# Kernel tuning notes

Measured on AMD Instinct MI355X. Metric: run time of the kernel, lower is better.

## Reference

```python
import jax, jax.numpy as jnp
import numpy as np

D_MODEL = 512
N_HEAD = 8
D_HEAD = D_MODEL // N_HEAD


def setup_inputs() -> dict:
    key = jax.random.key(0)
    ks = jax.random.split(key, 8)
    B, S, T = 4, 512, 32
    src = jax.random.normal(ks[0], (B, S, D_MODEL), dtype=jnp.float32)
    tgt = jax.random.normal(ks[1], (B, S, T, D_MODEL), dtype=jnp.float32)
    tgt_padding_mask = jax.random.bernoulli(ks[2], 0.1, (B, S, T))
    scale = 1.0 / np.sqrt(D_MODEL)
    in_proj_weight = jax.random.uniform(ks[3], (3 * D_MODEL, D_MODEL), dtype=jnp.float32, minval=-scale, maxval=scale)
    in_proj_bias = jnp.zeros((3 * D_MODEL,), dtype=jnp.float32)
    out_proj_weight = jax.random.uniform(ks[4], (D_MODEL, D_MODEL), dtype=jnp.float32, minval=-scale, maxval=scale)
    out_proj_bias = jnp.zeros((D_MODEL,), dtype=jnp.float32)
    return {
        "src": src,
        "tgt": tgt,
        "tgt_padding_mask": tgt_padding_mask,
        "in_proj_weight": in_proj_weight,
        "in_proj_bias": in_proj_bias,
        "out_proj_weight": out_proj_weight,
        "out_proj_bias": out_proj_bias,
    }


def reference(src, tgt, tgt_padding_mask, in_proj_weight, in_proj_bias, out_proj_weight, out_proj_bias):
    # KNN-style cross attention branch (tgt is [B, S, T, D]).
    B, S, _ = src.shape
    T = tgt.shape[-2]
    w_src, w_tgt = in_proj_weight[:D_MODEL], in_proj_weight[D_MODEL:]
    b_src, b_tgt = in_proj_bias[:D_MODEL], in_proj_bias[D_MODEL:]

    q = src @ w_src.T + b_src                      # [B, S, D]
    kv = tgt @ w_tgt.T + b_tgt                     # [B, S, T, 2D]
    k, v = kv[..., :D_MODEL], kv[..., D_MODEL:]

    # mask handling: drop the mask for queries with no valid tgt, zero them later
    attn_invalid = tgt_padding_mask                # [B, S, T]
    mask_no_tgt_valid = jnp.all(attn_invalid, axis=-1)           # [B, S]
    attn_invalid = attn_invalid & ~mask_no_tgt_valid[..., None]

    q = q.reshape(B, S, N_HEAD, D_HEAD)            # [B, S, H, Dh]
    k = k.reshape(B, S, T, N_HEAD, D_HEAD)
    v = v.reshape(B, S, T, N_HEAD, D_HEAD)

    attn = jnp.einsum("bshd,bsthd->bhst", q, k)    # [B, H, S, T]
    attn = jnp.where(attn_invalid[:, None], -jnp.inf, attn)
    attn = jax.nn.softmax(attn / jnp.sqrt(jnp.asarray(D_HEAD, attn.dtype)), axis=-1)

    out = jnp.einsum("bhst,bsthd->bshd", attn, v).reshape(B, S, D_MODEL)
    out = out @ out_proj_weight.T + out_proj_bias
    out = jnp.where(mask_no_tgt_valid[..., None], 0.0, out)
    return out
```

## Files before the change

kernel.cpp:

```cpp
#include <hip/hip_runtime.h>
#include <hip/hip_bf16.h>


typedef __attribute__((ext_vector_type(8))) short frag8;
typedef __attribute__((ext_vector_type(4))) float f32x4;

__device__ __forceinline__ short f2s(float v) {
    return __builtin_bit_cast(short, __float2bfloat16(v));
}
__device__ __forceinline__ float s2f(short x) {
    return __builtin_bit_cast(float, (unsigned)(unsigned short)x << 16);
}
__device__ __forceinline__ void stv(float* p, float v)          { *p = v; }
__device__ __forceinline__ void stv(__hip_bfloat16* p, float v) { *p = __float2bfloat16(v); }

__device__ __forceinline__ void gl_lds16(const __hip_bfloat16* g, __hip_bfloat16* l) {
    __builtin_amdgcn_global_load_lds(
        (const __attribute__((address_space(1))) unsigned int*)g,
        (__attribute__((address_space(3))) unsigned int*)l, 16, 0, 0);
}

__global__ __launch_bounds__(256)
void k_prep(const float* __restrict__ ipw, const float* __restrict__ opw,
            const float* __restrict__ src,
            __hip_bfloat16* __restrict__ ipw_bf, __hip_bfloat16* __restrict__ opw_bf,
            __hip_bfloat16* __restrict__ src_bf, __hip_bfloat16* __restrict__ Tk)
{
    __shared__ short tile[64][65];
    int b = blockIdx.x, tid = threadIdx.x;
#pragma unroll
    for (int i = 0; i < 4; ++i) {
        int g = b * 1024 + i * 256 + tid;
        const float4* in; ushort4* o4; int off;
        if (g < 196608)      { in = (const float4*)ipw; o4 = (ushort4*)ipw_bf; off = g; }
        else if (g < 262144) { in = (const float4*)opw; o4 = (ushort4*)opw_bf; off = g - 196608; }
        else                 { in = (const float4*)src; o4 = (ushort4*)src_bf; off = g - 262144; }
        float4 v = in[off];
        ushort4 o;
        o.x = (unsigned short)f2s(v.x); o.y = (unsigned short)f2s(v.y);
        o.z = (unsigned short)f2s(v.z); o.w = (unsigned short)f2s(v.w);
        o4[off] = o;
    }
    if (b < 128) {
        int bx = b & 15, by = b >> 4;
        const float* sp = ipw + (size_t)512 * 512;
#pragma unroll
        for (int i = 0; i < 16; ++i) {
            int idx = i * 256 + tid;
            int r = idx >> 6, c = idx & 63;
            tile[r][c] = f2s(sp[(size_t)(bx * 64 + r) * 512 + by * 64 + c]);
        }
        __syncthreads();
        short* Tks = (short*)Tk;
#pragma unroll
        for (int i = 0; i < 16; ++i) {
            int idx = i * 256 + tid;
            int rr = idx >> 6, cc = idx & 63;
            Tks[(size_t)(by * 64 + rr) * 1024 + bx * 64 + cc] = tile[cc][rr];
        }
    }
}

template<typename OUTT>
__device__ __forceinline__
void gemm64_dev(const __hip_bfloat16* __restrict__ A, const __hip_bfloat16* __restrict__ W,
                const float* __restrict__ bias, OUTT* __restrict__ C,
                const int* __restrict__ zmask,
                int N, int K, int tm, int tn, char* smem, int tid)
{
    short* sA = (short*)smem;
    short* sB = sA + 4096;
    int lane = tid & 63, w = tid >> 6;
    int wm = w >> 1, wn = w & 1;
    const __hip_bfloat16* Ab = A + (size_t)tm * 64 * K;
    const __hip_bfloat16* Wb = W + (size_t)tn * 64 * K;

    f32x4 acc[2][2];
#pragma unroll
    for (int i = 0; i < 2; ++i)
#pragma unroll
        for (int j = 0; j < 2; ++j) acc[i][j] = {0.f, 0.f, 0.f, 0.f};

    int wbase = (tid & ~63) * 8;
    int m = lane & 15, q = lane >> 4;
    int sw = (m & 7) * 8;
    int trow = tid >> 3;
    int tcb  = ((tid & 7) ^ (trow & 7)) * 8;

    for (int k0 = 0; k0 < K; k0 += 64) {
        gl_lds16(Ab + (size_t)trow * K + k0 + tcb,        (__hip_bfloat16*)&sA[wbase]);
        gl_lds16(Ab + (size_t)(32 + trow) * K + k0 + tcb, (__hip_bfloat16*)&sA[2048 + wbase]);
        gl_lds16(Wb + (size_t)trow * K + k0 + tcb,        (__hip_bfloat16*)&sB[wbase]);
        gl_lds16(Wb + (size_t)(32 + trow) * K + k0 + tcb, (__hip_bfloat16*)&sB[2048 + wbase]);
        __syncthreads();
#pragma unroll
        for (int ki = 0; ki < 2; ++ki) {
            frag8 af[2], bf2[2];
#pragma unroll
            for (int i = 0; i < 2; ++i)
                af[i] = *(const frag8*)&sA[(wm * 32 + i * 16 + m) * 64 + ((ki * 32 + q * 8) ^ sw)];
#pragma unroll
            for (int j = 0; j < 2; ++j)
                bf2[j] = *(const frag8*)&sB[(wn * 32 + j * 16 + m) * 64 + ((ki * 32 + q * 8) ^ sw)];
#pragma unroll
            for (int i = 0; i < 2; ++i)
#pragma unroll
                for (int j = 0; j < 2; ++j)
                    acc[i][j] = __builtin_amdgcn_mfma_f32_16x16x32_bf16(
                        af[i], bf2[j], acc[i][j], 0, 0, 0);
        }
        __syncthreads();
    }

    int rb = q * 4;
    bool zr[2][4] = {{false,false,false,false},{false,false,false,false}};
    if (zmask) {
#pragma unroll
        for (int i = 0; i < 2; ++i)
#pragma unroll
            for (int t = 0; t < 4; ++t) {
                int row = tm * 64 + wm * 32 + i * 16 + rb + t;
                const uint4* mp = (const uint4*)(zmask + (size_t)row * 32);
                unsigned a = 0xffffffffu;
#pragma unroll
                for (int u = 0; u < 8; ++u) { uint4 v = mp[u]; a &= v.x & v.y & v.z & v.w; }
                zr[i][t] = (a != 0u);
            }
    }
#pragma unroll
    for (int j = 0; j < 2; ++j) {
        int   col = tn * 64 + wn * 32 + j * 16 + m;
        float bv  = bias[col];
#pragma unroll
        for (int i = 0; i < 2; ++i) {
            int row0 = tm * 64 + wm * 32 + i * 16 + rb;
#pragma unroll
            for (int t = 0; t < 4; ++t) {
                float v = acc[i][j][t] + bv;
                if (zr[i][t]) v = 0.f;
                stv(&C[(size_t)(row0 + t) * N + col], v);
            }
        }
    }
}

__device__ __forceinline__
void gemm_bt_wave(const __hip_bfloat16* __restrict__ A, int lda,
                  const __hip_bfloat16* __restrict__ W, int ldw,
                  const float* __restrict__ bias, int bc0,
                  __hip_bfloat16* __restrict__ C, int ldc,
                  int K, int tm, int tn, int lane)
{
    int r  = lane & 15;
    int kq = (lane >> 4) << 3;
    const __hip_bfloat16* Ap = A + (size_t)(tm * 32 + r) * lda + kq;
    const __hip_bfloat16* Wp = W + (size_t)(tn * 32 + r) * ldw + kq;

    f32x4 acc[2][2];
#pragma unroll
    for (int i = 0; i < 2; ++i)
#pragma unroll
        for (int j = 0; j < 2; ++j) acc[i][j] = {0.f, 0.f, 0.f, 0.f};

    for (int k0 = 0; k0 < K; k0 += 32) {
        frag8 a[2], b[2];
#pragma unroll
        for (int i = 0; i < 2; ++i) a[i] = *(const frag8*)(Ap + (size_t)i * 16 * lda + k0);
#pragma unroll
        for (int j = 0; j < 2; ++j) b[j] = *(const frag8*)(Wp + (size_t)j * 16 * ldw + k0);
#pragma unroll
        for (int i = 0; i < 2; ++i)
#pragma unroll
            for (int j = 0; j < 2; ++j)
                acc[i][j] = __builtin_amdgcn_mfma_f32_16x16x32_bf16(a[i], b[j], acc[i][j], 0, 0, 0);
    }

    int rb = (lane >> 4) * 4;
#pragma unroll
    for (int j = 0; j < 2; ++j) {
        int   col = tn * 32 + j * 16 + r;
        float bv  = bias ? bias[bc0 + col] : 0.f;
#pragma unroll
        for (int i = 0; i < 2; ++i) {
            int row0 = tm * 32 + i * 16 + rb;
#pragma unroll
            for (int t = 0; t < 4; ++t)
                C[(size_t)(row0 + t) * ldc + col] = __float2bfloat16(acc[i][j][t] + bv);
        }
    }
}

__global__ __launch_bounds__(256)
void k_q(const __hip_bfloat16* src_bf, const __hip_bfloat16* ipw_bf,
         const float* ipb, __hip_bfloat16* q_bf)
{
    __shared__ __align__(16) char smem[16384];
    int b = blockIdx.x;
    gemm64_dev<__hip_bfloat16>(src_bf, ipw_bf, ipb, q_bf, nullptr,
                               512, 512, b >> 3, b & 7, smem, threadIdx.x);
}

__global__ __launch_bounds__(256)
void k_qk(const __hip_bfloat16* q_bf, const __hip_bfloat16* Tk, __hip_bfloat16* qkh)
{
    int tid = threadIdx.x;
    int t = blockIdx.x * 4 + (tid >> 6);
    int z = t >> 10, loc = t & 1023;
    gemm_bt_wave(q_bf + z * 64, 512, Tk + z * 64, 1024, nullptr, 0,
                 qkh + (size_t)z * 512, 4096, 64, loc >> 4, loc & 15, tid & 63);
}

__global__ __launch_bounds__(256)
void k_attn(const float* __restrict__ tgt,
            const __hip_bfloat16* __restrict__ qkh,
            const int* __restrict__ mask,
            __hip_bfloat16* __restrict__ tbar)
{
    int bs   = blockIdx.x;
    int tid  = threadIdx.x;
    int lane = tid & 63;
    int wv   = tid >> 6;
    int m    = lane & 15;
    int g4   = lane >> 4;

    __shared__ short sS[32 * 520];
    __shared__ short sQK[8 * 520];
    __shared__ int   sM[32];

    const float* tg = tgt + (size_t)bs * 32 * 512;
#pragma unroll
    for (int i = 0; i < 16; ++i) {
        int idx = i * 256 + tid;
        int row = idx >> 7, c4 = (idx & 127) * 4;
        float4 v = *(const float4*)(tg + (size_t)row * 512 + c4);
        ushort4 o;
        o.x = (unsigned short)f2s(v.x); o.y = (unsigned short)f2s(v.y);
        o.z = (unsigned short)f2s(v.z); o.w = (unsigned short)f2s(v.w);
        *(ushort4*)&sS[row * 520 + c4] = o;
    }
    const ushort4* qk4 = (const ushort4*)(qkh + (size_t)bs * 4096);
#pragma unroll
    for (int i = 0; i < 4; ++i) {
        int u = i * 256 + tid;
        int h = u >> 7, c4 = (u & 127) * 4;
        *(ushort4*)&sQK[h * 520 + c4] = qk4[u];
    }
    if (tid < 32) sM[tid] = mask[bs * 32 + tid];
    __syncthreads();

    int mk0 = sM[m], mk1 = sM[16 + m];
    bool allm = __all((mk0 != 0) && (mk1 != 0));

    f32x4 acc0 = {0.f,0.f,0.f,0.f}, acc1 = {0.f,0.f,0.f,0.f};
    {
        const short* qb  = &sQK[(m & 7) * 520 + g4 * 8];
        const short* t0p = &sS[m * 520 + g4 * 8];
        const short* t1p = t0p + 16 * 520;
#pragma unroll
        for (int k0 = 0; k0 < 512; k0 += 32) {
            frag8 af = *(const frag8*)(qb + k0);
            frag8 b0 = *(const frag8*)(t0p + k0);
            frag8 b1 = *(const frag8*)(t1p + k0);
            acc0 = __builtin_amdgcn_mfma_f32_16x16x32_bf16(af, b0, acc0, 0, 0, 0);
            acc1 = __builtin_amdgcn_mfma_f32_16x16x32_bf16(af, b1, acc1, 0, 0, 0);
        }
    }

    float p0v[4], p1v[4];
#pragma unroll
    for (int r = 0; r < 4; ++r) {
        float s0 = acc0[r] * 0.125f, s1 = acc1[r] * 0.125f;
        if (!allm) {
            if (mk0) s0 = -__builtin_inff();
            if (mk1) s1 = -__builtin_inff();
        }
        float mx = fmaxf(s0, s1);
#pragma unroll
        for (int off = 1; off < 16; off <<= 1) mx = fmaxf(mx, __shfl_xor(mx, off));
        float e0 = __expf(s0 - mx), e1 = __expf(s1 - mx);
        float sm = e0 + e1;
#pragma unroll
        for (int off = 1; off < 16; off <<= 1) sm += __shfl_xor(sm, off);
        float inv = 1.f / sm;
        p0v[r] = e0 * inv; p1v[r] = e1 * inv;
    }
    __syncthreads();

    short* sPw = sQK + wv * 512;
    if (g4 < 2) {
#pragma unroll
        for (int r = 0; r < 4; ++r) {
            int h = g4 * 4 + r;
            short h0 = f2s(p0v[r]), h1 = f2s(p1v[r]);
            sPw[h * 32 + m]            = h0;
            sPw[h * 32 + 16 + m]       = h1;
            sPw[256 + h * 32 + m]      = f2s(p0v[r] - s2f(h0));
            sPw[256 + h * 32 + 16 + m] = f2s(p1v[r] - s2f(h1));
        }
    }
    __syncthreads();
    frag8 paH = *(const frag8*)(sPw + (m & 7) * 32 + g4 * 8);
    frag8 paL = *(const frag8*)(sPw + 256 + (m & 7) * 32 + g4 * 8);
    __syncthreads();

    short* sO = sQK;
#pragma unroll
    for (int ci = 0; ci < 8; ++ci) {
        int cg = wv * 8 + ci;
        int cbase = cg * 16 + m;
        frag8 vb;
#pragma unroll
        for (int j = 0; j < 8; ++j)
            vb[j] = sS[(g4 * 8 + j) * 520 + cbase];
        f32x4 d = {0.f,0.f,0.f,0.f};
        d = __builtin_amdgcn_mfma_f32_16x16x32_bf16(paH, vb, d, 0, 0, 0);
        d = __builtin_amdgcn_mfma_f32_16x16x32_bf16(paL, vb, d, 0, 0, 0);
        if (g4 < 2) {
#pragma unroll
            for (int r = 0; r < 4; ++r)
                sO[(g4 * 4 + r) * 512 + cg * 16 + m] = f2s(d[r]);
        }
    }
    __syncthreads();

    ushort4* dst = (ushort4*)(tbar + (size_t)bs * 4096);
    const ushort4* so4 = (const ushort4*)sO;
#pragma unroll
    for (int i = 0; i < 4; ++i)
        dst[i * 256 + tid] = so4[i * 256 + tid];
}

__global__ __launch_bounds__(256)
void k_ao(const __hip_bfloat16* tbar, const __hip_bfloat16* ipw_bf,
          const float* ipb, __hip_bfloat16* ao_bf)
{
    int tid = threadIdx.x;
    int gw = blockIdx.x * 4 + (tid >> 6);
    int z = gw >> 7, loc = gw & 127;
    gemm_bt_wave(tbar + (size_t)z * 512, 4096,
                 ipw_bf + (size_t)(1024 + z * 64) * 512, 512,
                 ipb + 1024, z * 64, ao_bf + z * 64, 512, 512,
                 loc >> 1, loc & 1, tid & 63);
}

__global__ __launch_bounds__(256)
void k_out(const __hip_bfloat16* ao_bf, const __hip_bfloat16* opw_bf,
           const float* opb, float* out, const int* mask)
{
    __shared__ __align__(16) char smem[16384];
    int b = blockIdx.x;
    gemm64_dev<float>(ao_bf, opw_bf, opb, out, mask,
                      512, 512, b >> 3, b & 7, smem, threadIdx.x);
}

extern "C" void kernel_launch(void* const* d_in, const int* in_sizes, int n_in,
                              void* d_out, int out_size, void* d_ws, size_t ws_size,
                              hipStream_t stream)
{
    const float* src  = (const float*)d_in[0];
    const float* tgt  = (const float*)d_in[1];
    const int*   mask = (const int*)d_in[2];
    const float* ipw  = (const float*)d_in[3];
    const float* ipb  = (const float*)d_in[4];
    const float* opw  = (const float*)d_in[5];
    const float* opb  = (const float*)d_in[6];
    float*       out  = (float*)d_out;

    char* ws = (char*)d_ws;
    __hip_bfloat16* src_bf = (__hip_bfloat16*)(ws);
    __hip_bfloat16* ipw_bf = (__hip_bfloat16*)(ws + ((size_t)2 << 20));
    __hip_bfloat16* opw_bf = (__hip_bfloat16*)(ws + ((size_t)2 << 20) + 1536 * 512 * 2);
    __hip_bfloat16* q_bf   = (__hip_bfloat16*)(ws + ((size_t)4 << 20));
    __hip_bfloat16* Tk     = (__hip_bfloat16*)(ws + ((size_t)6 << 20));
    __hip_bfloat16* qkh    = (__hip_bfloat16*)(ws + ((size_t)8 << 20));
    __hip_bfloat16* tbar   = (__hip_bfloat16*)(ws + ((size_t)24 << 20));
    __hip_bfloat16* ao_bf  = (__hip_bfloat16*)(ws + ((size_t)40 << 20));

    k_prep<<<512, 256, 0, stream>>>(ipw, opw, src, ipw_bf, opw_bf, src_bf, Tk);
    k_q   <<<256, 256, 0, stream>>>(src_bf, ipw_bf, ipb, q_bf);
    k_qk  <<<2048, 256, 0, stream>>>(q_bf, Tk, qkh);
    k_attn<<<2048, 256, 0, stream>>>(tgt, qkh, mask, tbar);
    k_ao  <<<256, 256, 0, stream>>>(tbar, ipw_bf, ipb, ao_bf);
    k_out <<<256, 256, 0, stream>>>(ao_bf, opw_bf, opb, out, mask);
}
```

Baseline: 252.7 us.

## Fuse fp32-to-bf16 conversion into GEMM loaders and drop prep kernel

Removes the separate prep kernel that converted weights and src to bf16. The GEMMs now load fp32 operands and convert them to bf16 on the fly into LDS or registers, and the Tk transpose moves into the Q-projection kernel. The qk kernel also stages its output tile through LDS so it can write coalesced 8-byte vectors. This saves one launch and a global round trip, at the cost of doubled fp32 read traffic inside the GEMM loops and synchronous loads in place of direct-to-LDS loads.

```diff
diff --git a/kernel.cpp b/kernel.cpp
--- a/kernel.cpp
+++ b/kernel.cpp
@@ -20,78 +20,59 @@
         (__attribute__((address_space(3))) unsigned int*)l, 16, 0, 0);
 }
 
-__global__ __launch_bounds__(256)
-void k_prep(const float* __restrict__ ipw, const float* __restrict__ opw,
-            const float* __restrict__ src,
-            __hip_bfloat16* __restrict__ ipw_bf, __hip_bfloat16* __restrict__ opw_bf,
-            __hip_bfloat16* __restrict__ src_bf, __hip_bfloat16* __restrict__ Tk)
-{
-    __shared__ short tile[64][65];
-    int b = blockIdx.x, tid = threadIdx.x;
-#pragma unroll
-    for (int i = 0; i < 4; ++i) {
-        int g = b * 1024 + i * 256 + tid;
-        const float4* in; ushort4* o4; int off;
-        if (g < 196608)      { in = (const float4*)ipw; o4 = (ushort4*)ipw_bf; off = g; }
-        else if (g < 262144) { in = (const float4*)opw; o4 = (ushort4*)opw_bf; off = g - 196608; }
-        else                 { in = (const float4*)src; o4 = (ushort4*)src_bf; off = g - 262144; }
-        float4 v = in[off];
-        ushort4 o;
-        o.x = (unsigned short)f2s(v.x); o.y = (unsigned short)f2s(v.y);
-        o.z = (unsigned short)f2s(v.z); o.w = (unsigned short)f2s(v.w);
-        o4[off] = o;
-    }
-    if (b < 128) {
-        int bx = b & 15, by = b >> 4;
-        const float* sp = ipw + (size_t)512 * 512;
-#pragma unroll
-        for (int i = 0; i < 16; ++i) {
-            int idx = i * 256 + tid;
-            int r = idx >> 6, c = idx & 63;
-            tile[r][c] = f2s(sp[(size_t)(bx * 64 + r) * 512 + by * 64 + c]);
-        }
-        __syncthreads();
-        short* Tks = (short*)Tk;
-#pragma unroll
-        for (int i = 0; i < 16; ++i) {
-            int idx = i * 256 + tid;
-            int rr = idx >> 6, cc = idx & 63;
-            Tks[(size_t)(by * 64 + rr) * 1024 + bx * 64 + cc] = tile[cc][rr];
-        }
-    }
-}
-
-template<typename OUTT>
+__device__ __forceinline__ frag8 cvt8(const float* p) {
+    float4 u = *(const float4*)p, v = *(const float4*)(p + 4);
+    frag8 o = { f2s(u.x), f2s(u.y), f2s(u.z), f2s(u.w),
+                f2s(v.x), f2s(v.y), f2s(v.z), f2s(v.w) };
+    return o;
+}
+
+template<bool AF32, bool WF32, typename OUTT>
 __device__ __forceinline__
-void gemm64_dev(const __hip_bfloat16* __restrict__ A, const __hip_bfloat16* __restrict__ W,
-                const float* __restrict__ bias, OUTT* __restrict__ C,
-                const int* __restrict__ zmask,
-                int N, int K, int tm, int tn, char* smem, int tid)
+void gemm64x(const void* Aop, const void* Wop,
+             const float* __restrict__ bias, OUTT* __restrict__ C,
+             const int* __restrict__ zmask,
+             int N, int K, int tm, int tn, char* smem, int tid)
 {
     short* sA = (short*)smem;
     short* sB = sA + 4096;
     int lane = tid & 63, w = tid >> 6;
     int wm = w >> 1, wn = w & 1;
-    const __hip_bfloat16* Ab = A + (size_t)tm * 64 * K;
-    const __hip_bfloat16* Wb = W + (size_t)tn * 64 * K;
-
-    f32x4 acc[2][2];
-#pragma unroll
-    for (int i = 0; i < 2; ++i)
-#pragma unroll
-        for (int j = 0; j < 2; ++j) acc[i][j] = {0.f, 0.f, 0.f, 0.f};
-
-    int wbase = (tid & ~63) * 8;
     int m = lane & 15, q = lane >> 4;
     int sw = (m & 7) * 8;
     int trow = tid >> 3;
     int tcb  = ((tid & 7) ^ (trow & 7)) * 8;
+    int wbase = (tid & ~63) * 8;
+
+    f32x4 acc[2][2];
+#pragma unroll
+    for (int i = 0; i < 2; ++i)
+#pragma unroll
+        for (int j = 0; j < 2; ++j) acc[i][j] = {0.f, 0.f, 0.f, 0.f};
 
     for (int k0 = 0; k0 < K; k0 += 64) {
-        gl_lds16(Ab + (size_t)trow * K + k0 + tcb,        (__hip_bfloat16*)&sA[wbase]);
-        gl_lds16(Ab + (size_t)(32 + trow) * K + k0 + tcb, (__hip_bfloat16*)&sA[2048 + wbase]);
-        gl_lds16(Wb + (size_t)trow * K + k0 + tcb,        (__hip_bfloat16*)&sB[wbase]);
-        gl_lds16(Wb + (size_t)(32 + trow) * K + k0 + tcb, (__hip_bfloat16*)&sB[2048 + wbase]);
+        if constexpr (AF32) {
+            const float* Af = (const float*)Aop + (size_t)tm * 64 * K;
+#pragma unroll
+            for (int s = 0; s < 2; ++s)
+                *(frag8*)&sA[s * 2048 + tid * 8] =
+                    cvt8(Af + (size_t)(s * 32 + trow) * K + k0 + tcb);
+        } else {
+            const __hip_bfloat16* Ab = (const __hip_bfloat16*)Aop + (size_t)tm * 64 * K;
+            gl_lds16(Ab + (size_t)trow * K + k0 + tcb,        (__hip_bfloat16*)&sA[wbase]);
+            gl_lds16(Ab + (size_t)(32 + trow) * K + k0 + tcb, (__hip_bfloat16*)&sA[2048 + wbase]);
+        }
+        if constexpr (WF32) {
+            const float* Wf = (const float*)Wop + (size_t)tn * 64 * K;
+#pragma unroll
+            for (int s = 0; s < 2; ++s)
+                *(frag8*)&sB[s * 2048 + tid * 8] =
+                    cvt8(Wf + (size_t)(s * 32 + trow) * K + k0 + tcb);
+        } else {
+            const __hip_bfloat16* Wb = (const __hip_bfloat16*)Wop + (size_t)tn * 64 * K;
+            gl_lds16(Wb + (size_t)trow * K + k0 + tcb,        (__hip_bfloat16*)&sB[wbase]);
+            gl_lds16(Wb + (size_t)(32 + trow) * K + k0 + tcb, (__hip_bfloat16*)&sB[2048 + wbase]);
+        }
         __syncthreads();
 #pragma unroll
         for (int ki = 0; ki < 2; ++ki) {
@@ -144,17 +125,51 @@
     }
 }
 
-__device__ __forceinline__
-void gemm_bt_wave(const __hip_bfloat16* __restrict__ A, int lda,
-                  const __hip_bfloat16* __restrict__ W, int ldw,
-                  const float* __restrict__ bias, int bc0,
-                  __hip_bfloat16* __restrict__ C, int ldc,
-                  int K, int tm, int tn, int lane)
-{
-    int r  = lane & 15;
-    int kq = (lane >> 4) << 3;
-    const __hip_bfloat16* Ap = A + (size_t)(tm * 32 + r) * lda + kq;
-    const __hip_bfloat16* Wp = W + (size_t)(tn * 32 + r) * ldw + kq;
+__global__ __launch_bounds__(256)
+void k_q(const float* __restrict__ src, const float* __restrict__ ipw,
+         const float* __restrict__ ipb, __hip_bfloat16* __restrict__ q_bf,
+         __hip_bfloat16* __restrict__ Tk)
+{
+    __shared__ __align__(16) char smem[16384];
+    int b = blockIdx.x, tid = threadIdx.x;
+    gemm64x<true, true, __hip_bfloat16>(src, ipw, ipb, q_bf, nullptr,
+                                        512, 512, b >> 3, b & 7, smem, tid);
+    if (b < 128) {
+        __syncthreads();
+        short (*tile)[65] = (short(*)[65])smem;
+        int bx = b & 15, by = b >> 4;
+        const float* sp = ipw + (size_t)512 * 512;
+#pragma unroll
+        for (int i = 0; i < 16; ++i) {
+            int idx = i * 256 + tid;
+            int r = idx >> 6, c = idx & 63;
+            tile[r][c] = f2s(sp[(size_t)(bx * 64 + r) * 512 + by * 64 + c]);
+        }
+        __syncthreads();
+        short* Tks = (short*)Tk;
+#pragma unroll
+        for (int i = 0; i < 16; ++i) {
+            int idx = i * 256 + tid;
+            int rr = idx >> 6, cc = idx & 63;
+            Tks[(size_t)(by * 64 + rr) * 1024 + bx * 64 + cc] = tile[cc][rr];
+        }
+    }
+}
+
+__global__ __launch_bounds__(256)
+void k_qk(const __hip_bfloat16* __restrict__ q_bf,
+          const __hip_bfloat16* __restrict__ Tk,
+          __hip_bfloat16* __restrict__ qkh)
+{
+    __shared__ short sO[32 * 132];
+    int tid = threadIdx.x, wv = tid >> 6, lane = tid & 63;
+    int t   = blockIdx.x * 4 + wv;
+    int z   = t >> 10, loc = t & 1023;
+    int tm  = loc >> 4, tn = loc & 15;
+    int r   = lane & 15, kq = (lane >> 4) << 3;
+
+    const __hip_bfloat16* Ap = q_bf + (size_t)z * 64 + (size_t)(tm * 32 + r) * 512 + kq;
+    const __hip_bfloat16* Wp = Tk  + (size_t)z * 64 + (size_t)(tn * 32 + r) * 1024 + kq;
 
     f32x4 acc[2][2];
 #pragma unroll
@@ -162,52 +177,40 @@
 #pragma unroll
         for (int j = 0; j < 2; ++j) acc[i][j] = {0.f, 0.f, 0.f, 0.f};
 
-    for (int k0 = 0; k0 < K; k0 += 32) {
-        frag8 a[2], b[2];
-#pragma unroll
-        for (int i = 0; i < 2; ++i) a[i] = *(const frag8*)(Ap + (size_t)i * 16 * lda + k0);
-#pragma unroll
-        for (int j = 0; j < 2; ++j) b[j] = *(const frag8*)(Wp + (size_t)j * 16 * ldw + k0);
+#pragma unroll
+    for (int k0 = 0; k0 < 64; k0 += 32) {
+        frag8 a[2], bb[2];
+#pragma unroll
+        for (int i = 0; i < 2; ++i) a[i]  = *(const frag8*)(Ap + (size_t)i * 16 * 512 + k0);
+#pragma unroll
+        for (int j = 0; j < 2; ++j) bb[j] = *(const frag8*)(Wp + (size_t)j * 16 * 1024 + k0);
 #pragma unroll
         for (int i = 0; i < 2; ++i)
 #pragma unroll
             for (int j = 0; j < 2; ++j)
-                acc[i][j] = __builtin_amdgcn_mfma_f32_16x16x32_bf16(a[i], b[j], acc[i][j], 0, 0, 0);
+                acc[i][j] = __builtin_amdgcn_mfma_f32_16x16x32_bf16(a[i], bb[j], acc[i][j], 0, 0, 0);
     }
 
     int rb = (lane >> 4) * 4;
 #pragma unroll
-    for (int j = 0; j < 2; ++j) {
-        int   col = tn * 32 + j * 16 + r;
-        float bv  = bias ? bias[bc0 + col] : 0.f;
-#pragma unroll
-        for (int i = 0; i < 2; ++i) {
-            int row0 = tm * 32 + i * 16 + rb;
-#pragma unroll
-            for (int t = 0; t < 4; ++t)
-                C[(size_t)(row0 + t) * ldc + col] = __float2bfloat16(acc[i][j][t] + bv);
-        }
-    }
-}
-
-__global__ __launch_bounds__(256)
-void k_q(const __hip_bfloat16* src_bf, const __hip_bfloat16* ipw_bf,
-         const float* ipb, __hip_bfloat16* q_bf)
-{
-    __shared__ __align__(16) char smem[16384];
-    int b = blockIdx.x;
-    gemm64_dev<__hip_bfloat16>(src_bf, ipw_bf, ipb, q_bf, nullptr,
-                               512, 512, b >> 3, b & 7, smem, threadIdx.x);
-}
-
-__global__ __launch_bounds__(256)
-void k_qk(const __hip_bfloat16* q_bf, const __hip_bfloat16* Tk, __hip_bfloat16* qkh)
-{
-    int tid = threadIdx.x;
-    int t = blockIdx.x * 4 + (tid >> 6);
-    int z = t >> 10, loc = t & 1023;
-    gemm_bt_wave(q_bf + z * 64, 512, Tk + z * 64, 1024, nullptr, 0,
-                 qkh + (size_t)z * 512, 4096, 64, loc >> 4, loc & 15, tid & 63);
+    for (int j = 0; j < 2; ++j)
+#pragma unroll
+        for (int i = 0; i < 2; ++i)
+#pragma unroll
+            for (int tq = 0; tq < 4; ++tq)
+                sO[(i * 16 + rb + tq) * 132 + wv * 32 + j * 16 + r] = f2s(acc[i][j][tq]);
+    __syncthreads();
+
+    int tb  = blockIdx.x * 4;
+    int zb  = tb >> 10, locb = tb & 1023;
+    int tmb = locb >> 4, tnb = locb & 15;
+#pragma unroll
+    for (int i = 0; i < 4; ++i) {
+        int u = i * 256 + tid;
+        int lr = u >> 5, c4 = (u & 31) * 4;
+        *(ushort4*)&qkh[(size_t)(tmb * 32 + lr) * 4096 + zb * 512 + tnb * 32 + c4] =
+            *(const ushort4*)&sO[lr * 132 + c4];
+    }
 }
 
 __global__ __launch_bounds__(256)
@@ -331,26 +334,62 @@
 }
 
 __global__ __launch_bounds__(256)
-void k_ao(const __hip_bfloat16* tbar, const __hip_bfloat16* ipw_bf,
-          const float* ipb, __hip_bfloat16* ao_bf)
-{
-    int tid = threadIdx.x;
+void k_ao(const __hip_bfloat16* __restrict__ tbar, const float* __restrict__ ipw,
+          const float* __restrict__ ipb, __hip_bfloat16* __restrict__ ao_bf)
+{
+    int tid = threadIdx.x, lane = tid & 63;
     int gw = blockIdx.x * 4 + (tid >> 6);
     int z = gw >> 7, loc = gw & 127;
-    gemm_bt_wave(tbar + (size_t)z * 512, 4096,
-                 ipw_bf + (size_t)(1024 + z * 64) * 512, 512,
-                 ipb + 1024, z * 64, ao_bf + z * 64, 512, 512,
-                 loc >> 1, loc & 1, tid & 63);
+    int tm = loc >> 1, tn = loc & 1;
+    int r = lane & 15, kq = (lane >> 4) << 3;
+
+    const __hip_bfloat16* Ap = tbar + (size_t)z * 512 + (size_t)(tm * 32 + r) * 4096 + kq;
+    const float*          Wp = ipw + (size_t)(1024 + z * 64 + tn * 32 + r) * 512 + kq;
+
+    f32x4 acc[2][2];
+#pragma unroll
+    for (int i = 0; i < 2; ++i)
+#pragma unroll
+        for (int j = 0; j < 2; ++j) acc[i][j] = {0.f, 0.f, 0.f, 0.f};
+
+    for (int k0 = 0; k0 < 512; k0 += 32) {
+        frag8 a[2], bb[2];
+#pragma unroll
+        for (int i = 0; i < 2; ++i) a[i] = *(const frag8*)(Ap + (size_t)i * 16 * 4096 + k0);
+#pragma unroll
+        for (int j = 0; j < 2; ++j) bb[j] = cvt8(Wp + (size_t)j * 16 * 512 + k0);
+#pragma unroll
+        for (int i = 0; i < 2; ++i)
+#pragma unroll
+            for (int j = 0; j < 2; ++j)
+                acc[i][j] = __builtin_amdgcn_mfma_f32_16x16x32_bf16(a[i], bb[j], acc[i][j], 0, 0, 0);
+    }
+
+    int rb = (lane >> 4) * 4;
+#pragma unroll
+    for (int j = 0; j < 2; ++j) {
+        int   col = tn * 32 + j * 16 + r;
+        float bv  = ipb[1024 + z * 64 + col];
+#pragma unroll
+        for (int i = 0; i < 2; ++i) {
+            int row0 = tm * 32 + i * 16 + rb;
+#pragma unroll
+            for (int t = 0; t < 4; ++t)
+                ao_bf[(size_t)(row0 + t) * 512 + z * 64 + col] =
+                    __float2bfloat16(acc[i][j][t] + bv);
+        }
+    }
 }
 
 __global__ __launch_bounds__(256)
-void k_out(const __hip_bfloat16* ao_bf, const __hip_bfloat16* opw_bf,
-           const float* opb, float* out, const int* mask)
+void k_out(const __hip_bfloat16* __restrict__ ao_bf, const float* __restrict__ opw,
+           const float* __restrict__ opb, float* __restrict__ out,
+           const int* __restrict__ mask)
 {
     __shared__ __align__(16) char smem[16384];
     int b = blockIdx.x;
-    gemm64_dev<float>(ao_bf, opw_bf, opb, out, mask,
-                      512, 512, b >> 3, b & 7, smem, threadIdx.x);
+    gemm64x<false, true, float>(ao_bf, opw, opb, out, mask,
+                                512, 512, b >> 3, b & 7, smem, threadIdx.x);
 }
 
 extern "C" void kernel_launch(void* const* d_in, const int* in_sizes, int n_in,
@@ -367,19 +406,15 @@
     float*       out  = (float*)d_out;
 
     char* ws = (char*)d_ws;
-    __hip_bfloat16* src_bf = (__hip_bfloat16*)(ws);
-    __hip_bfloat16* ipw_bf = (__hip_bfloat16*)(ws + ((size_t)2 << 20));
-    __hip_bfloat16* opw_bf = (__hip_bfloat16*)(ws + ((size_t)2 << 20) + 1536 * 512 * 2);
     __hip_bfloat16* q_bf   = (__hip_bfloat16*)(ws + ((size_t)4 << 20));
     __hip_bfloat16* Tk     = (__hip_bfloat16*)(ws + ((size_t)6 << 20));
     __hip_bfloat16* qkh    = (__hip_bfloat16*)(ws + ((size_t)8 << 20));
     __hip_bfloat16* tbar   = (__hip_bfloat16*)(ws + ((size_t)24 << 20));
     __hip_bfloat16* ao_bf  = (__hip_bfloat16*)(ws + ((size_t)40 << 20));
 
-    k_prep<<<512, 256, 0, stream>>>(ipw, opw, src, ipw_bf, opw_bf, src_bf, Tk);
-    k_q   <<<256, 256, 0, stream>>>(src_bf, ipw_bf, ipb, q_bf);
+    k_q   <<<256,  256, 0, stream>>>(src, ipw, ipb, q_bf, Tk);
     k_qk  <<<2048, 256, 0, stream>>>(q_bf, Tk, qkh);
     k_attn<<<2048, 256, 0, stream>>>(tgt, qkh, mask, tbar);
-    k_ao  <<<256, 256, 0, stream>>>(tbar, ipw_bf, ipb, ao_bf);
-    k_out <<<256, 256, 0, stream>>>(ao_bf, opw_bf, opb, out, mask);
-}
+    k_ao  <<<256,  256, 0, stream>>>(tbar, ipw, ipb, ao_bf);
+    k_out <<<256,  256, 0, stream>>>(ao_bf, opw, opb, out, mask);
+}
```

After: 264.0 us. 1.04x slower.
